# Kernel tuning notes

Measured on AMD Instinct MI355X. Metric: run time of the kernel, lower is better.

The kernel has to match this reference:

```python
import jax, jax.numpy as jnp
import numpy as np

E = 100000
VERTEX_DIM = 64
EDGE_DIM = 128
MESSAGE_DIM = 64


def setup_inputs() -> dict:
    key = jax.random.key(0)
    k1, k2, k3, k4 = jax.random.split(key, 4)
    vertices = jax.random.normal(k1, (E, VERTEX_DIM), dtype=jnp.float32)
    edges = jax.random.normal(k2, (E, EDGE_DIM), dtype=jnp.float32)
    # nn.Linear(edge_dim, message_dim * vertex_dim): weight [out, in], bias [out]
    W = jax.random.normal(k3, (MESSAGE_DIM * VERTEX_DIM, EDGE_DIM), dtype=jnp.float32) * (1.0 / np.sqrt(EDGE_DIM))
    b = jax.random.normal(k4, (MESSAGE_DIM * VERTEX_DIM,), dtype=jnp.float32) * 0.01
    return {"vertices": vertices, "edges": edges, "W": W, "b": b}


def reference(vertices, edges, W, b):
    # edge_net(edges): [E, message_dim*vertex_dim]
    proj = edges @ W.T + b
    # view to [E, message_dim, vertex_dim], then batched matvec with vertices [E, vertex_dim]
    proj = proj.reshape(edges.shape[0], MESSAGE_DIM, VERTEX_DIM)
    message = jnp.einsum('emv,ev->em', proj, vertices)  # [E, message_dim]
    return message
```

## Files before the change

kernel.cpp:

```cpp
#include <hip/hip_runtime.h>
#include <hip/hip_bf16.h>
#include <stdint.h>


typedef __attribute__((ext_vector_type(8))) short bf16x8;
typedef __attribute__((ext_vector_type(4))) float f32x4;

#define MSG_D 64
#define VTX_D 64
#define EDG_D 128
#define EPB 128

__device__ __forceinline__ unsigned pk_bf16_trunc(float lo, float hi) {
  return __builtin_amdgcn_perm(__float_as_uint(hi), __float_as_uint(lo), 0x07060302u);
}

__global__ void prep_bf16(const float* __restrict__ W, const float* __restrict__ b,
                          __hip_bfloat16* __restrict__ Wb, __hip_bfloat16* __restrict__ bb,
                          int nW, int nb) {
  int i = blockIdx.x * blockDim.x + threadIdx.x;
  if (i < nW) {
    Wb[i] = __float2bfloat16(W[i]);
  } else {
    int j = i - nW;
    if (j < nb) bb[j] = __float2bfloat16(b[j]);
  }
}

__global__ void __launch_bounds__(256)
edge_msg_mfma(const float* __restrict__ Vtx, const float* __restrict__ Xe,
              const __hip_bfloat16* __restrict__ Wb, const __hip_bfloat16* __restrict__ bb,
              float* __restrict__ out, int E)
{
  __shared__ unsigned short lds[2][64 * 128];

  const int tid  = threadIdx.x;
  const int lane = tid & 63;
  const int wv   = tid >> 6;
  const int q    = lane >> 4;
  const int ln   = lane & 15;

  const int ebase = blockIdx.x * EPB + wv * 32;

  float4 xa[2][4], xb[2][4];
  const float* vr[2];
  #pragma unroll
  for (int t = 0; t < 2; ++t) {
    int e  = ebase + 16 * t + ln;
    int er = e < E ? e : (E - 1);
    const float* xrow = Xe + (size_t)er * EDG_D;
    #pragma unroll
    for (int s = 0; s < 4; ++s) {
      int c = s * 32 + q * 8;
      xa[t][s] = *(const float4*)(xrow + c);
      xb[t][s] = *(const float4*)(xrow + c + 4);
    }
    vr[t] = Vtx + (size_t)er * VTX_D;
  }

  f32x4 acc[2][4];
  #pragma unroll
  for (int t = 0; t < 2; ++t)
    #pragma unroll
    for (int n = 0; n < 4; ++n)
      acc[t][n] = (f32x4){0.f, 0.f, 0.f, 0.f};

  const int srow   = tid >> 2;
  const int schunk = tid & 3;
  const unsigned short* wbase = (const unsigned short*)Wb + (size_t)srow * 8192 + schunk * 32;
  int sdst[4];
  #pragma unroll
  for (int j = 0; j < 4; ++j) {
    int c  = schunk * 4 + j;
    int cp = (c & 8) | ((c ^ (srow & 7)) & 7);
    sdst[j] = srow * 128 + cp * 8;
  }

  int rcp[4];
  #pragma unroll
  for (int s = 0; s < 4; ++s) {
    int c  = s * 4 + q;
    rcp[s] = (c & 8) | ((c ^ (ln & 7)) & 7);
  }

  {
    #pragma unroll
    for (int j = 0; j < 4; ++j) {
      uint4 r = *(const uint4*)(wbase + j * 8);
      *(uint4*)(&lds[0][sdst[j]]) = r;
    }
  }
  float vv0 = vr[0][0];
  float vv1 = vr[1][0];
  __syncthreads();

  for (int v = 0; v < 64; ++v) {
    uint4 r0, r1, r2, r3;
    float nv0 = vv0, nv1 = vv1;
    const bool more = (v < 63);
    if (more) {
      const unsigned short* g = wbase + (size_t)(v + 1) * 128;
      r0 = *(const uint4*)(g + 0);
      r1 = *(const uint4*)(g + 8);
      r2 = *(const uint4*)(g + 16);
      r3 = *(const uint4*)(g + 24);
      nv0 = vr[0][v + 1];
      nv1 = vr[1][v + 1];
    }

    const unsigned short* buf = &lds[v & 1][0];
    #pragma unroll
    for (int s = 0; s < 4; ++s) {
      union { bf16x8 v8; unsigned u[4]; } af0, af1;
      {
        float4 a = xa[0][s], b2 = xb[0][s];
        af0.u[0] = pk_bf16_trunc(vv0 * a.x,  vv0 * a.y);
        af0.u[1] = pk_bf16_trunc(vv0 * a.z,  vv0 * a.w);
        af0.u[2] = pk_bf16_trunc(vv0 * b2.x, vv0 * b2.y);
        af0.u[3] = pk_bf16_trunc(vv0 * b2.z, vv0 * b2.w);
      }
      {
        float4 a = xa[1][s], b2 = xb[1][s];
        af1.u[0] = pk_bf16_trunc(vv1 * a.x,  vv1 * a.y);
        af1.u[1] = pk_bf16_trunc(vv1 * a.z,  vv1 * a.w);
        af1.u[2] = pk_bf16_trunc(vv1 * b2.x, vv1 * b2.y);
        af1.u[3] = pk_bf16_trunc(vv1 * b2.z, vv1 * b2.w);
      }
      const unsigned short* pbase = buf + ln * 128 + rcp[s] * 8;
      #pragma unroll
      for (int n = 0; n < 4; ++n) {
        const bf16x8 bf = *(const bf16x8*)(pbase + n * 2048);
        acc[0][n] = __builtin_amdgcn_mfma_f32_16x16x32_bf16(af0.v8, bf, acc[0][n], 0, 0, 0);
        acc[1][n] = __builtin_amdgcn_mfma_f32_16x16x32_bf16(af1.v8, bf, acc[1][n], 0, 0, 0);
      }
    }

    if (more) {
      unsigned short* p = &lds[(v + 1) & 1][0];
      *(uint4*)(p + sdst[0]) = r0;
      *(uint4*)(p + sdst[1]) = r1;
      *(uint4*)(p + sdst[2]) = r2;
      *(uint4*)(p + sdst[3]) = r3;
    }
    __syncthreads();
    vv0 = nv0; vv1 = nv1;
  }

  #pragma unroll
  for (int s = 0; s < 2; ++s) {
    union { bf16x8 v8; unsigned u[4]; } af0, af1;
    {
      float4 a  = *(const float4*)(vr[0] + s * 32 + q * 8);
      float4 b2 = *(const float4*)(vr[0] + s * 32 + q * 8 + 4);
      af0.u[0] = pk_bf16_trunc(a.x,  a.y);
      af0.u[1] = pk_bf16_trunc(a.z,  a.w);
      af0.u[2] = pk_bf16_trunc(b2.x, b2.y);
      af0.u[3] = pk_bf16_trunc(b2.z, b2.w);
    }
    {
      float4 a  = *(const float4*)(vr[1] + s * 32 + q * 8);
      float4 b2 = *(const float4*)(vr[1] + s * 32 + q * 8 + 4);
      af1.u[0] = pk_bf16_trunc(a.x,  a.y);
      af1.u[1] = pk_bf16_trunc(a.z,  a.w);
      af1.u[2] = pk_bf16_trunc(b2.x, b2.y);
      af1.u[3] = pk_bf16_trunc(b2.z, b2.w);
    }
    #pragma unroll
    for (int n = 0; n < 4; ++n) {
      int m = n * 16 + ln;
      const bf16x8 bf = *(const bf16x8*)((const char*)bb + ((size_t)m * 64 + s * 32 + q * 8) * 2);
      acc[0][n] = __builtin_amdgcn_mfma_f32_16x16x32_bf16(af0.v8, bf, acc[0][n], 0, 0, 0);
      acc[1][n] = __builtin_amdgcn_mfma_f32_16x16x32_bf16(af1.v8, bf, acc[1][n], 0, 0, 0);
    }
  }

  #pragma unroll
  for (int t = 0; t < 2; ++t) {
    #pragma unroll
    for (int r = 0; r < 4; ++r) {
      int e = ebase + 16 * t + 4 * q + r;
      if (e < E) {
        float* orow = out + (size_t)e * MSG_D;
        #pragma unroll
        for (int n = 0; n < 4; ++n)
          orow[n * 16 + ln] = acc[t][n][r];
      }
    }
  }
}

__global__ void edge_msg_naive(const float* __restrict__ Vtx, const float* __restrict__ Xe,
                               const float* __restrict__ W, const float* __restrict__ b,
                               float* __restrict__ out, int E) {
  __shared__ float xs[EDG_D];
  __shared__ float vs[VTX_D];
  int e = blockIdx.x;
  int m = threadIdx.x;
  for (int i = m; i < EDG_D; i += 64) xs[i] = Xe[(size_t)e * EDG_D + i];
  for (int i = m; i < VTX_D; i += 64) vs[i] = Vtx[(size_t)e * VTX_D + i];
  __syncthreads();
  float s = 0.f;
  for (int v = 0; v < VTX_D; ++v) {
    const float* wr = W + (size_t)(m * 64 + v) * EDG_D;
    float p = b[m * 64 + v];
    for (int k = 0; k < EDG_D; ++k) p += xs[k] * wr[k];
    s += p * vs[v];
  }
  out[(size_t)e * MSG_D + m] = s;
}

extern "C" void kernel_launch(void* const* d_in, const int* in_sizes, int n_in,
                              void* d_out, int out_size, void* d_ws, size_t ws_size,
                              hipStream_t stream) {
  const float* Vtx = (const float*)d_in[0];
  const float* Xe  = (const float*)d_in[1];
  const float* W   = (const float*)d_in[2];
  const float* b   = (const float*)d_in[3];
  float* out = (float*)d_out;

  const int E  = in_sizes[0] / VTX_D;
  const int nW = in_sizes[2];
  const int nb = in_sizes[3];
  const size_t need = (size_t)(nW + nb) * sizeof(__hip_bfloat16);

  if (ws_size < need) {
    edge_msg_naive<<<E, 64, 0, stream>>>(Vtx, Xe, W, b, out, E);
    return;
  }

  __hip_bfloat16* Wb = (__hip_bfloat16*)d_ws;
  __hip_bfloat16* bb = Wb + nW;

  int nTot = nW + nb;
  prep_bf16<<<(nTot + 255) / 256, 256, 0, stream>>>(W, b, Wb, bb, nW, nb);

  int blocks = (E + EPB - 1) / EPB;
  edge_msg_mfma<<<blocks, 256, 0, stream>>>(Vtx, Xe, Wb, bb, out, E);
}
```

Baseline: 251.4 us.

## Switch to f16 MFMA with direct-to-LDS weight loads and 2x2 wave tiling

Replaces the bf16 pipeline with f16. W is pre-swizzled into a per-v tiled layout in the prep kernel so the main kernel can stream weight slices straight into LDS with global_load_lds. Waves are rearranged into a 2x2 grid of 64 edges by 32 outputs, and edge features are converted to f16 once so the per-step scaling uses packed f16 multiplies instead of repeated f32 multiply and pack. The aim is to cut VALU conversion work and register-staged LDS stores. The risks are f16 range and precision loss when the vertex-scaled products are rounded, and a hard-coded weight-size check that falls back to the naive kernel otherwise.

Result: slower. 283.5 us (+12.8%).

```diff
diff --git a/kernel.cpp b/kernel.cpp
--- a/kernel.cpp
+++ b/kernel.cpp
@@ -3,7 +3,9 @@
 #include <stdint.h>
 
 
-typedef __attribute__((ext_vector_type(8))) short bf16x8;
+typedef _Float16 f16;
+typedef __attribute__((ext_vector_type(2))) _Float16 f16x2;
+typedef __attribute__((ext_vector_type(8))) _Float16 f16x8;
 typedef __attribute__((ext_vector_type(4))) float f32x4;
 
 #define MSG_D 64
@@ -11,179 +13,153 @@
 #define EDG_D 128
 #define EPB 128
 
-__device__ __forceinline__ unsigned pk_bf16_trunc(float lo, float hi) {
-  return __builtin_amdgcn_perm(__float_as_uint(hi), __float_as_uint(lo), 0x07060302u);
-}
-
-__global__ void prep_bf16(const float* __restrict__ W, const float* __restrict__ b,
-                          __hip_bfloat16* __restrict__ Wb, __hip_bfloat16* __restrict__ bb,
-                          int nW, int nb) {
-  int i = blockIdx.x * blockDim.x + threadIdx.x;
-  if (i < nW) {
-    Wb[i] = __float2bfloat16(W[i]);
-  } else {
-    int j = i - nW;
-    if (j < nb) bb[j] = __float2bfloat16(b[j]);
-  }
-}
-
-__global__ void __launch_bounds__(256)
-edge_msg_mfma(const float* __restrict__ Vtx, const float* __restrict__ Xe,
-              const __hip_bfloat16* __restrict__ Wb, const __hip_bfloat16* __restrict__ bb,
-              float* __restrict__ out, int E)
+__device__ __forceinline__ void dma16(const void* g, void* l) {
+  __builtin_amdgcn_global_load_lds(
+      (const __attribute__((address_space(1))) unsigned int*)g,
+      (__attribute__((address_space(3))) unsigned int*)l, 16, 0, 0);
+}
+
+__global__ void prep_f16(const float* __restrict__ W, const float* __restrict__ b,
+                         f16* __restrict__ Wh, f16* __restrict__ bh) {
+  int tid = blockIdx.x * 256 + threadIdx.x;
+  int c = tid & 15, m = (tid >> 4) & 63, v = tid >> 10;
+  const float* src = W + ((size_t)(m * 64 + v) * 128 + c * 8);
+  int cp = (c & 8) | ((c ^ (m & 7)) & 7);
+  f16* dst = Wh + ((size_t)v * 8192 + m * 128 + cp * 8);
+  float4 a = *(const float4*)src;
+  float4 d = *(const float4*)(src + 4);
+  f16x8 h = {(f16)a.x, (f16)a.y, (f16)a.z, (f16)a.w,
+             (f16)d.x, (f16)d.y, (f16)d.z, (f16)d.w};
+  *(f16x8*)dst = h;
+  if (tid < 4096) bh[tid] = (f16)b[tid];
+}
+
+__global__ __launch_bounds__(256, 3) void edge_msg_f16(
+    const float* __restrict__ Vtx, const float* __restrict__ Xe,
+    const f16* __restrict__ Wh, const f16* __restrict__ bh,
+    float* __restrict__ out, int E)
 {
-  __shared__ unsigned short lds[2][64 * 128];
+  __shared__ __align__(16) f16 lds[2][8192];
 
   const int tid  = threadIdx.x;
   const int lane = tid & 63;
   const int wv   = tid >> 6;
+  const int wm   = wv & 1;
+  const int wn   = wv >> 1;
   const int q    = lane >> 4;
   const int ln   = lane & 15;
-
-  const int ebase = blockIdx.x * EPB + wv * 32;
-
-  float4 xa[2][4], xb[2][4];
-  const float* vr[2];
-  #pragma unroll
-  for (int t = 0; t < 2; ++t) {
-    int e  = ebase + 16 * t + ln;
+  const int eoff = blockIdx.x * EPB + wm * 64;
+
+  f16x8 xh[4][4];
+  const float* vrow[4];
+  #pragma unroll
+  for (int t = 0; t < 4; ++t) {
+    int e  = eoff + 16 * t + ln;
     int er = e < E ? e : (E - 1);
-    const float* xrow = Xe + (size_t)er * EDG_D;
+    const float* xr = Xe + (size_t)er * EDG_D;
     #pragma unroll
     for (int s = 0; s < 4; ++s) {
-      int c = s * 32 + q * 8;
-      xa[t][s] = *(const float4*)(xrow + c);
-      xb[t][s] = *(const float4*)(xrow + c + 4);
-    }
-    vr[t] = Vtx + (size_t)er * VTX_D;
-  }
-
-  f32x4 acc[2][4];
-  #pragma unroll
-  for (int t = 0; t < 2; ++t)
-    #pragma unroll
-    for (int n = 0; n < 4; ++n)
+      float4 a = *(const float4*)(xr + s * 32 + q * 8);
+      float4 d = *(const float4*)(xr + s * 32 + q * 8 + 4);
+      xh[t][s] = (f16x8){(f16)a.x, (f16)a.y, (f16)a.z, (f16)a.w,
+                         (f16)d.x, (f16)d.y, (f16)d.z, (f16)d.w};
+    }
+    vrow[t] = Vtx + (size_t)er * VTX_D;
+  }
+
+  f32x4 acc[4][2];
+  #pragma unroll
+  for (int t = 0; t < 4; ++t)
+    #pragma unroll
+    for (int n = 0; n < 2; ++n)
       acc[t][n] = (f32x4){0.f, 0.f, 0.f, 0.f};
 
-  const int srow   = tid >> 2;
-  const int schunk = tid & 3;
-  const unsigned short* wbase = (const unsigned short*)Wb + (size_t)srow * 8192 + schunk * 32;
-  int sdst[4];
-  #pragma unroll
-  for (int j = 0; j < 4; ++j) {
-    int c  = schunk * 4 + j;
-    int cp = (c & 8) | ((c ^ (srow & 7)) & 7);
-    sdst[j] = srow * 128 + cp * 8;
-  }
-
-  int rcp[4];
+  const char* wsrc = (const char*)Wh + wv * 4096 + lane * 16;
+  char* ldst[2] = { (char*)&lds[0][0] + wv * 4096, (char*)&lds[1][0] + wv * 4096 };
+
+  int rb[4];
   #pragma unroll
   for (int s = 0; s < 4; ++s) {
     int c  = s * 4 + q;
-    rcp[s] = (c & 8) | ((c ^ (ln & 7)) & 7);
-  }
-
-  {
-    #pragma unroll
-    for (int j = 0; j < 4; ++j) {
-      uint4 r = *(const uint4*)(wbase + j * 8);
-      *(uint4*)(&lds[0][sdst[j]]) = r;
-    }
-  }
-  float vv0 = vr[0][0];
-  float vv1 = vr[1][0];
+    int cp = (c & 8) | ((c ^ (ln & 7)) & 7);
+    rb[s] = ln * 256 + cp * 16;
+  }
+
+  #pragma unroll
+  for (int i = 0; i < 4; ++i) dma16(wsrc + i * 1024, ldst[0] + i * 1024);
+  float vv[4], nv[4];
+  #pragma unroll
+  for (int t = 0; t < 4; ++t) vv[t] = vrow[t][0];
   __syncthreads();
 
   for (int v = 0; v < 64; ++v) {
-    uint4 r0, r1, r2, r3;
-    float nv0 = vv0, nv1 = vv1;
     const bool more = (v < 63);
     if (more) {
-      const unsigned short* g = wbase + (size_t)(v + 1) * 128;
-      r0 = *(const uint4*)(g + 0);
-      r1 = *(const uint4*)(g + 8);
-      r2 = *(const uint4*)(g + 16);
-      r3 = *(const uint4*)(g + 24);
-      nv0 = vr[0][v + 1];
-      nv1 = vr[1][v + 1];
-    }
-
-    const unsigned short* buf = &lds[v & 1][0];
+      const char* g = wsrc + (size_t)(v + 1) * 16384;
+      char* l = ldst[(v + 1) & 1];
+      #pragma unroll
+      for (int i = 0; i < 4; ++i) dma16(g + i * 1024, l + i * 1024);
+      #pragma unroll
+      for (int t = 0; t < 4; ++t) nv[t] = vrow[t][v + 1];
+    }
+
+    f16x2 hh[4];
+    #pragma unroll
+    for (int t = 0; t < 4; ++t) { f16 h = (f16)vv[t]; hh[t] = (f16x2){h, h}; }
+
+    const char* bufb = (const char*)&lds[v & 1][0] + wn * 8192;
     #pragma unroll
     for (int s = 0; s < 4; ++s) {
-      union { bf16x8 v8; unsigned u[4]; } af0, af1;
-      {
-        float4 a = xa[0][s], b2 = xb[0][s];
-        af0.u[0] = pk_bf16_trunc(vv0 * a.x,  vv0 * a.y);
-        af0.u[1] = pk_bf16_trunc(vv0 * a.z,  vv0 * a.w);
-        af0.u[2] = pk_bf16_trunc(vv0 * b2.x, vv0 * b2.y);
-        af0.u[3] = pk_bf16_trunc(vv0 * b2.z, vv0 * b2.w);
+      f16x8 bf0 = *(const f16x8*)(bufb + rb[s]);
+      f16x8 bf1 = *(const f16x8*)(bufb + rb[s] + 4096);
+      #pragma unroll
+      for (int t = 0; t < 4; ++t) {
+        union { f16x2 h2[4]; f16x8 v8; } af;
+        union { f16x8 v8; f16x2 h2[4]; } xs;
+        xs.v8 = xh[t][s];
+        af.h2[0] = hh[t] * xs.h2[0];
+        af.h2[1] = hh[t] * xs.h2[1];
+        af.h2[2] = hh[t] * xs.h2[2];
+        af.h2[3] = hh[t] * xs.h2[3];
+        acc[t][0] = __builtin_amdgcn_mfma_f32_16x16x32_f16(af.v8, bf0, acc[t][0], 0, 0, 0);
+        acc[t][1] = __builtin_amdgcn_mfma_f32_16x16x32_f16(af.v8, bf1, acc[t][1], 0, 0, 0);
       }
-      {
-        float4 a = xa[1][s], b2 = xb[1][s];
-        af1.u[0] = pk_bf16_trunc(vv1 * a.x,  vv1 * a.y);
-        af1.u[1] = pk_bf16_trunc(vv1 * a.z,  vv1 * a.w);
-        af1.u[2] = pk_bf16_trunc(vv1 * b2.x, vv1 * b2.y);
-        af1.u[3] = pk_bf16_trunc(vv1 * b2.z, vv1 * b2.w);
-      }
-      const unsigned short* pbase = buf + ln * 128 + rcp[s] * 8;
-      #pragma unroll
-      for (int n = 0; n < 4; ++n) {
-        const bf16x8 bf = *(const bf16x8*)(pbase + n * 2048);
-        acc[0][n] = __builtin_amdgcn_mfma_f32_16x16x32_bf16(af0.v8, bf, acc[0][n], 0, 0, 0);
-        acc[1][n] = __builtin_amdgcn_mfma_f32_16x16x32_bf16(af1.v8, bf, acc[1][n], 0, 0, 0);
-      }
-    }
-
-    if (more) {
-      unsigned short* p = &lds[(v + 1) & 1][0];
-      *(uint4*)(p + sdst[0]) = r0;
-      *(uint4*)(p + sdst[1]) = r1;
-      *(uint4*)(p + sdst[2]) = r2;
-      *(uint4*)(p + sdst[3]) = r3;
     }
     __syncthreads();
-    vv0 = nv0; vv1 = nv1;
+    #pragma unroll
+    for (int t = 0; t < 4; ++t) vv[t] = nv[t];
   }
 
   #pragma unroll
   for (int s = 0; s < 2; ++s) {
-    union { bf16x8 v8; unsigned u[4]; } af0, af1;
-    {
-      float4 a  = *(const float4*)(vr[0] + s * 32 + q * 8);
-      float4 b2 = *(const float4*)(vr[0] + s * 32 + q * 8 + 4);
-      af0.u[0] = pk_bf16_trunc(a.x,  a.y);
-      af0.u[1] = pk_bf16_trunc(a.z,  a.w);
-      af0.u[2] = pk_bf16_trunc(b2.x, b2.y);
-      af0.u[3] = pk_bf16_trunc(b2.z, b2.w);
-    }
-    {
-      float4 a  = *(const float4*)(vr[1] + s * 32 + q * 8);
-      float4 b2 = *(const float4*)(vr[1] + s * 32 + q * 8 + 4);
-      af1.u[0] = pk_bf16_trunc(a.x,  a.y);
-      af1.u[1] = pk_bf16_trunc(a.z,  a.w);
-      af1.u[2] = pk_bf16_trunc(b2.x, b2.y);
-      af1.u[3] = pk_bf16_trunc(b2.z, b2.w);
-    }
-    #pragma unroll
-    for (int n = 0; n < 4; ++n) {
-      int m = n * 16 + ln;
-      const bf16x8 bf = *(const bf16x8*)((const char*)bb + ((size_t)m * 64 + s * 32 + q * 8) * 2);
-      acc[0][n] = __builtin_amdgcn_mfma_f32_16x16x32_bf16(af0.v8, bf, acc[0][n], 0, 0, 0);
-      acc[1][n] = __builtin_amdgcn_mfma_f32_16x16x32_bf16(af1.v8, bf, acc[1][n], 0, 0, 0);
-    }
-  }
-
-  #pragma unroll
-  for (int t = 0; t < 2; ++t) {
+    f16x8 av[4];
+    #pragma unroll
+    for (int t = 0; t < 4; ++t) {
+      const float* vr = vrow[t];
+      float4 a = *(const float4*)(vr + s * 32 + q * 8);
+      float4 d = *(const float4*)(vr + s * 32 + q * 8 + 4);
+      av[t] = (f16x8){(f16)a.x, (f16)a.y, (f16)a.z, (f16)a.w,
+                      (f16)d.x, (f16)d.y, (f16)d.z, (f16)d.w};
+    }
+    #pragma unroll
+    for (int n = 0; n < 2; ++n) {
+      int col = wn * 32 + n * 16 + ln;
+      f16x8 bf = *(const f16x8*)(bh + (size_t)col * 64 + s * 32 + q * 8);
+      #pragma unroll
+      for (int t = 0; t < 4; ++t)
+        acc[t][n] = __builtin_amdgcn_mfma_f32_16x16x32_f16(av[t], bf, acc[t][n], 0, 0, 0);
+    }
+  }
+
+  #pragma unroll
+  for (int t = 0; t < 4; ++t) {
     #pragma unroll
     for (int r = 0; r < 4; ++r) {
-      int e = ebase + 16 * t + 4 * q + r;
+      int e = eoff + 16 * t + 4 * q + r;
       if (e < E) {
-        float* orow = out + (size_t)e * MSG_D;
-        #pragma unroll
-        for (int n = 0; n < 4; ++n)
-          orow[n * 16 + ln] = acc[t][n][r];
+        float* orow = out + (size_t)e * MSG_D + wn * 32 + ln;
+        orow[0]  = acc[t][0][r];
+        orow[16] = acc[t][1][r];
       }
     }
   }
@@ -221,19 +197,18 @@
   const int E  = in_sizes[0] / VTX_D;
   const int nW = in_sizes[2];
   const int nb = in_sizes[3];
-  const size_t need = (size_t)(nW + nb) * sizeof(__hip_bfloat16);
-
-  if (ws_size < need) {
+  const size_t need = (size_t)(nW + nb) * sizeof(f16);
+
+  if (ws_size < need || nW != 524288) {
     edge_msg_naive<<<E, 64, 0, stream>>>(Vtx, Xe, W, b, out, E);
     return;
   }
 
-  __hip_bfloat16* Wb = (__hip_bfloat16*)d_ws;
-  __hip_bfloat16* bb = Wb + nW;
-
-  int nTot = nW + nb;
-  prep_bf16<<<(nTot + 255) / 256, 256, 0, stream>>>(W, b, Wb, bb, nW, nb);
+  f16* Wh = (f16*)d_ws;
+  f16* bh = Wh + nW;
+
+  prep_f16<<<256, 256, 0, stream>>>(W, b, Wh, bh);
 
   int blocks = (E + EPB - 1) / EPB;
-  edge_msg_mfma<<<blocks, 256, 0, stream>>>(Vtx, Xe, Wb, bb, out, E);
-}
+  edge_msg_f16<<<blocks, 256, 0, stream>>>(Vtx, Xe, Wh, bh, out, E);
+}
```
